# Performance work log

Hardware: AMD Instinct MI355X
Metric: run time of the kernel (lower is better)

Reference implementation:

```python
import jax, jax.numpy as jnp
import numpy as np

B, S, HID = 2, 2048, 1024
NH, HD = 4, 256
SCALE = HD ** -0.5


def _rope(x, fr, fi):
    # x: [B,S,NH,HD]; fr/fi: [S,HD//2]
    b, s, n, d = x.shape
    xr = x.reshape(b, s, n, d // 2, 2)
    re, im = xr[..., 0], xr[..., 1]
    fr = fr[None, :, None, :]
    fi = fi[None, :, None, :]
    rr = re * fr - im * fi
    ri = re * fi + im * fr
    return jnp.stack((rr, ri), axis=-1).reshape(b, s, n, d)


def setup_inputs() -> dict:
    key = jax.random.key(0)
    k1, k2, k3 = jax.random.split(key, 3)
    hidden_states = jax.random.normal(k1, (B, S, HID), dtype=jnp.float32)
    # RoPE frequencies (standard theta=10000)
    inv_freq = 1.0 / (10000.0 ** (np.arange(0, HD, 2, dtype=np.float32) / HD))  # [HD//2]
    t = np.arange(S, dtype=np.float32)
    ang = np.outer(t, inv_freq)  # [S, HD//2]
    freqs_real = jnp.asarray(np.cos(ang), dtype=jnp.float32)
    freqs_imag = jnp.asarray(np.sin(ang), dtype=jnp.float32)
    # causal additive mask [1,1,S,S]
    causal = jnp.tril(jnp.ones((S, S), dtype=bool))
    mask = jnp.where(causal, 0.0, -1e9).astype(jnp.float32)[None, None]
    W_qkv = jax.random.normal(k2, (3 * HID, HID), dtype=jnp.float32) * (HID ** -0.5)
    W_o = jax.random.normal(k3, (HID, HID), dtype=jnp.float32) * (HID ** -0.5)
    return {"hidden_states": hidden_states, "freqs_real": freqs_real,
            "freqs_imag": freqs_imag, "mask": mask, "W_qkv": W_qkv, "W_o": W_o}


def reference(hidden_states, freqs_real, freqs_imag, mask, W_qkv, W_o):
    b, s, _ = hidden_states.shape
    qkv = hidden_states @ W_qkv.T  # [B,S,3*HID]
    qkv = qkv.reshape(b, s, 3, NH, HD)
    q, k, v = qkv[:, :, 0], qkv[:, :, 1], qkv[:, :, 2]
    q = _rope(q, freqs_real, freqs_imag)
    k = _rope(k, freqs_real, freqs_imag)
    scores = jnp.einsum('bqhd,bkhd->bhqk', q * SCALE, k) + mask  # [B,NH,S,S]
    probs = jax.nn.softmax(scores, axis=-1)
    attn = jnp.einsum('bhqk,bkhd->bqhd', probs, v).reshape(b, s, HID)
    return attn @ W_o.T
```

## Files before the change

### kernel.cpp

```cpp
#include <hip/hip_runtime.h>
#include <stdint.h>

#define NB 2
#define NS 2048
#define NHID 1024
#define NHEADS 4
#define DHEAD 256
#define NP 128
#define QK_SCALE 0.0625f

typedef unsigned short ushort_t;
typedef __bf16 bf16x8 __attribute__((ext_vector_type(8)));
typedef float floatx4 __attribute__((ext_vector_type(4)));
typedef short shortx8 __attribute__((ext_vector_type(8)));
typedef unsigned short ushortx4 __attribute__((ext_vector_type(4)));
typedef unsigned short ushortx8 __attribute__((ext_vector_type(8)));

__device__ __forceinline__ float bf2f(ushort_t u) {
    unsigned int x = ((unsigned int)u) << 16;
    return __builtin_bit_cast(float, x);
}
__device__ __forceinline__ ushort_t f2bf(float f) {
    unsigned int u = __builtin_bit_cast(unsigned int, f);
    u += 0x7fff + ((u >> 16) & 1);
    return (ushort_t)(u >> 16);
}

__device__ __forceinline__ floatx4 mfma16(bf16x8 a, bf16x8 b, floatx4 c) {
    return __builtin_amdgcn_mfma_f32_16x16x32_bf16(a, b, c, 0, 0, 0);
}

__device__ __forceinline__ void gload_lds16(const void* g, void* l) {
    __builtin_amdgcn_global_load_lds(
        (const __attribute__((address_space(1))) void*)g,
        (__attribute__((address_space(3))) void*)l, 16, 0, 0);
}

#define N4_H (4096 * 1024 / 4)
#define N4_WQ (3072 * 1024 / 4)
#define N4_WO (1024 * 1024 / 4)
__global__ __launch_bounds__(256) void cast3_kernel(const float* __restrict__ inH,
                                                    const float* __restrict__ inWq,
                                                    const float* __restrict__ inWo,
                                                    ushort_t* __restrict__ out) {
    int i = blockIdx.x * 256 + threadIdx.x;
    const float* src;
    int j = i;
    if (i < N4_H) {
        src = inH;
    } else if (i < N4_H + N4_WQ) {
        src = inWq; j = i - N4_H;
    } else {
        src = inWo; j = i - (N4_H + N4_WQ);
    }
    float4 v = ((const float4*)src)[j];
    ushortx4 o = { f2bf(v.x), f2bf(v.y), f2bf(v.z), f2bf(v.w) };
    ((ushortx4*)out)[i] = o;
}


__global__ __launch_bounds__(256) void gemm_bt_f32s(const ushort_t* __restrict__ A,
                                                    const ushort_t* __restrict__ Bt,
                                                    float* __restrict__ C0,
                                                    float* __restrict__ C1,
                                                    int M, int N, int K) {
    __shared__ ushort_t sA[4][128 * 32];
    __shared__ ushort_t sB[4][128 * 32];
    const int t = threadIdx.x;
    const int f = blockIdx.x;
    const int xcd = f & 7;
    const int idx = f >> 3;
    const int im = idx >> 4;
    const int in = (idx >> 1) & 7;
    const int kz = idx & 1;
    const int m0 = (xcd * 4 + im) * 128;
    const int n0 = in * 128;
    float* Cout = kz ? C1 : C0;
    const int kbeg = kz * (K / 2);
    const int w = t >> 6, l = t & 63;
    const int wm = (w >> 1) * 64, wn = (w & 1) * 64;
    const int lc = l & 15, lq = l >> 4;

    floatx4 acc[4][4];
#pragma unroll
    for (int i = 0; i < 4; i++)
#pragma unroll
        for (int j = 0; j < 4; j++) acc[i][j] = (floatx4){0.f, 0.f, 0.f, 0.f};

    const int srow = w * 16 + (l >> 2);
    const int scol = (((l & 3) - (l >> 2)) & 3) * 8;
    const ushort_t* Ag = A + (size_t)(m0 + srow) * K + scol + kbeg;
    const ushort_t* Bg = Bt + (size_t)(n0 + srow) * K + scol + kbeg;
    const int lofs = t * 8;

    auto stage = [&](int bsel, int kk) {
        ushort_t* lA = &sA[bsel][lofs];
        ushort_t* lB = &sB[bsel][lofs];
        gload_lds16(Ag + kk, lA);
        gload_lds16(Ag + kk + (size_t)64 * K, lA + 2048);
        gload_lds16(Bg + kk, lB);
        gload_lds16(Bg + kk + (size_t)64 * K, lB + 2048);
    };
    auto compute = [&](int bsel) {
        const ushort_t* cA = sA[bsel];
        const ushort_t* cB = sB[bsel];
        bf16x8 af[4], bfv[4];
#pragma unroll
        for (int i = 0; i < 4; i++) {
            int R = wm + i * 16 + lc;
            af[i] = *(const bf16x8*)&cA[R * 32 + ((lq + R) & 3) * 8];
        }
#pragma unroll
        for (int j = 0; j < 4; j++) {
            int R = wn + j * 16 + lc;
            bfv[j] = *(const bf16x8*)&cB[R * 32 + ((lq + R) & 3) * 8];
        }
#pragma unroll
        for (int i = 0; i < 4; i++)
#pragma unroll
            for (int j = 0; j < 4; j++)
                acc[i][j] = mfma16(af[i], bfv[j], acc[i][j]);
    };

    stage(0, 0); stage(1, 32); stage(2, 64);
#pragma unroll 1
    for (int s = 0; s <= 16 - 4; ++s) {
        asm volatile("s_waitcnt vmcnt(8)" ::: "memory");
        __builtin_amdgcn_sched_barrier(0);
        __builtin_amdgcn_s_barrier();
        compute(s & 3);
        stage((s + 3) & 3, (s + 3) * 32);
    }
    asm volatile("s_waitcnt vmcnt(8)" ::: "memory");
    __builtin_amdgcn_sched_barrier(0);
    __builtin_amdgcn_s_barrier();
    compute(13 & 3);
    asm volatile("s_waitcnt vmcnt(4)" ::: "memory");
    __builtin_amdgcn_sched_barrier(0);
    __builtin_amdgcn_s_barrier();
    compute(14 & 3);
    asm volatile("s_waitcnt vmcnt(0)" ::: "memory");
    __builtin_amdgcn_sched_barrier(0);
    __builtin_amdgcn_s_barrier();
    compute(15 & 3);

#pragma unroll
    for (int i = 0; i < 4; i++) {
        int row = m0 + wm + i * 16 + lq * 4;
#pragma unroll
        for (int j = 0; j < 4; j++) {
            int col = n0 + wn + j * 16 + lc;
#pragma unroll
            for (int r = 0; r < 4; r++)
                Cout[(size_t)(row + r) * N + col] = acc[i][j][r];
        }
    }
}

__global__ __launch_bounds__(256) void add_f32(const float* __restrict__ a,
                                               const float* __restrict__ b,
                                               float* __restrict__ o, int n4) {
    int i = blockIdx.x * 256 + threadIdx.x;
    if (i < n4) {
        float4 x = ((const float4*)a)[i];
        float4 y = ((const float4*)b)[i];
        float4 z = { x.x + y.x, x.y + y.y, x.z + y.z, x.w + y.w };
        ((float4*)o)[i] = z;
    }
}

__global__ __launch_bounds__(256) void gemm_qkv(const ushort_t* __restrict__ A,
                                                const ushort_t* __restrict__ Bt,
                                                const float* __restrict__ fre,
                                                const float* __restrict__ fim,
                                                ushort_t* __restrict__ Q,
                                                ushort_t* __restrict__ Kk,
                                                ushort_t* __restrict__ Vt) {
    const int M_K = 1024;
    __shared__ ushort_t sA[4][128 * 32];
    __shared__ ushort_t sB[4][128 * 32];
    const int t = threadIdx.x;
    const int f = blockIdx.x;
    const int xcd = f & 7;
    const int idx = f >> 3;
    const int mr = xcd & 3, nr = xcd >> 2;
    const int im = idx & 7, in = idx >> 3;
    const int m0 = (mr * 8 + im) * 128;
    const int n0 = (nr * 12 + in) * 128;
    const int w = t >> 6, l = t & 63;
    const int wm = (w >> 1) * 64, wn = (w & 1) * 64;
    const int lc = l & 15, lq = l >> 4;

    floatx4 acc[4][4];
#pragma unroll
    for (int i = 0; i < 4; i++)
#pragma unroll
        for (int j = 0; j < 4; j++) acc[i][j] = (floatx4){0.f, 0.f, 0.f, 0.f};

    const int srow = w * 16 + (l >> 2);
    const int scol = (((l & 3) - (l >> 2)) & 3) * 8;
    const ushort_t* Ag = A + (size_t)(m0 + srow) * M_K + scol;
    const ushort_t* Bg = Bt + (size_t)(n0 + srow) * M_K + scol;
    const int lofs = t * 8;

    auto stage = [&](int bsel, int kk) {
        ushort_t* lA = &sA[bsel][lofs];
        ushort_t* lB = &sB[bsel][lofs];
        gload_lds16(Ag + kk, lA);
        gload_lds16(Ag + kk + (size_t)64 * M_K, lA + 2048);
        gload_lds16(Bg + kk, lB);
        gload_lds16(Bg + kk + (size_t)64 * M_K, lB + 2048);
    };
    auto compute = [&](int bsel) {
        const ushort_t* cA = sA[bsel];
        const ushort_t* cB = sB[bsel];
        bf16x8 af[4], bfv[4];
#pragma unroll
        for (int i = 0; i < 4; i++) {
            int R = wm + i * 16 + lc;
            af[i] = *(const bf16x8*)&cA[R * 32 + ((lq + R) & 3) * 8];
        }
#pragma unroll
        for (int j = 0; j < 4; j++) {
            int R = wn + j * 16 + lc;
            bfv[j] = *(const bf16x8*)&cB[R * 32 + ((lq + R) & 3) * 8];
        }
#pragma unroll
        for (int i = 0; i < 4; i++)
#pragma unroll
            for (int j = 0; j < 4; j++)
                acc[i][j] = mfma16(af[i], bfv[j], acc[i][j]);
    };

    stage(0, 0); stage(1, 32); stage(2, 64);
#pragma unroll 1
    for (int s = 0; s <= 32 - 4; ++s) {
        asm volatile("s_waitcnt vmcnt(8)" ::: "memory");
        __builtin_amdgcn_sched_barrier(0);
        __builtin_amdgcn_s_barrier();
        compute(s & 3);
        stage((s + 3) & 3, (s + 3) * 32);
    }
    asm volatile("s_waitcnt vmcnt(8)" ::: "memory");
    __builtin_amdgcn_sched_barrier(0);
    __builtin_amdgcn_s_barrier();
    compute(29 & 3);
    asm volatile("s_waitcnt vmcnt(4)" ::: "memory");
    __builtin_amdgcn_sched_barrier(0);
    __builtin_amdgcn_s_barrier();
    compute(30 & 3);
    asm volatile("s_waitcnt vmcnt(0)" ::: "memory");
    __builtin_amdgcn_sched_barrier(0);
    __builtin_amdgcn_s_barrier();
    compute(31 & 3);

    const int sect = n0 >> 10;
#pragma unroll
    for (int i = 0; i < 4; i++) {
        int row = m0 + wm + i * 16 + lq * 4;
        int b = row >> 11;
        int srow2 = row & 2047;
#pragma unroll
        for (int j = 0; j < 4; j++) {
            int col = n0 + wn + j * 16 + lc;
            int d = col & 255;
            int h = (col >> 8) & 3;
            int bh = b * NHEADS + h;
            if (sect == 2) {
                ushortx4 pack = { f2bf(acc[i][j][0]), f2bf(acc[i][j][1]),
                                  f2bf(acc[i][j][2]), f2bf(acc[i][j][3]) };
                *(ushortx4*)&Vt[((size_t)bh * 256 + d) * NS + srow2] = pack;
            } else {
                int p = d >> 1;
                int odd = d & 1;
                ushort_t* dst = (sect == 0) ? Q : Kk;
#pragma unroll
                for (int r = 0; r < 4; r++) {
                    float v = acc[i][j][r];
                    float vp = __shfl_xor(v, 1);
                    int s = srow2 + r;
                    float c = fre[s * NP + p], si = fim[s * NP + p];
                    float out = odd ? (vp * si + v * c) : (v * c - vp * si);
                    if (sect == 0) out *= QK_SCALE;
                    dst[((size_t)bh * NS + s) * DHEAD + d] = f2bf(out);
                }
            }
        }
    }
}

#define BQ3 128
#define BKV3 64
#define PPAD 72
#define CHCAP 6
#define NPART_BH 51
#define OPART_SPLIT 224

__global__ __launch_bounds__(256, 2) void flash_attn4(const ushort_t* __restrict__ Q,
                                                      const ushort_t* __restrict__ K,
                                                      const ushort_t* __restrict__ Vt,
                                                      ushort_t* __restrict__ OpA,
                                                      ushort_t* __restrict__ OpB,
                                                      float* __restrict__ ml) {
    __shared__ ushort_t sK[BKV3 * 256];
    __shared__ ushort_t sV[DHEAD * 64];
    __shared__ ushort_t sP[4][16 * PPAD];

    int rem = blockIdx.x, qt = 15, nsp;
    for (;;) {
        nsp = (2 * (qt + 1) + CHCAP - 1) / CHCAP;
        if (rem < nsp) break;
        rem -= nsp;
        qt--;
    }
    const int nch = 2 * (qt + 1);
    const int cbeg = rem * CHCAP;
    const int cend = (cbeg + CHCAP < nch) ? cbeg + CHCAP : nch;

    const int h = blockIdx.y, b = blockIdx.z;
    const int t = threadIdx.x, w = t >> 6, l = t & 63;
    const int lc = l & 15, lq = l >> 4;
    const int bh = b * NHEADS + h;
    const size_t base = (size_t)bh * NS * DHEAD;
    const int q0 = qt * BQ3;

    const int krb = w * 2 + (l >> 5);
    const int kck = ((l & 31) - (krb & 7)) & 31;
    const size_t koff = (size_t)krb * 256 + kck * 8;
    const int vrb = w * 8 + (l >> 3);
    const int vck = ((l & 7) - (vrb & 7)) & 7;
    const size_t voff = (size_t)vrb * NS + vck * 8;
    ushort_t* dK = &sK[w * 512 + l * 8];
    ushort_t* dV = &sV[w * 512 + l * 8];

    bf16x8 qf[2][8];
#pragma unroll
    for (int gq = 0; gq < 2; gq++) {
        const ushort_t* qrow = Q + base + (size_t)(q0 + w * 32 + gq * 16 + lc) * DHEAD + lq * 8;
#pragma unroll
        for (int dk = 0; dk < 8; dk++) qf[gq][dk] = *(const bf16x8*)(qrow + dk * 32);
    }

    floatx4 accO[2][16];
#pragma unroll
    for (int gq = 0; gq < 2; gq++)
#pragma unroll
        for (int j = 0; j < 16; j++) accO[gq][j] = (floatx4){0.f, 0.f, 0.f, 0.f};
    float lrun[2][4] = {{0.f, 0.f, 0.f, 0.f}, {0.f, 0.f, 0.f, 0.f}};

    for (int kc = cbeg; kc < cend; kc++) {
        const int kb = kc * BKV3;
        __syncthreads();
        {
            const ushort_t* ksrc = K + base + (size_t)kb * 256 + koff;
            const ushort_t* vsrc = Vt + base + kb + voff;
#pragma unroll
            for (int j = 0; j < 8; j++)
                gload_lds16(ksrc + j * (8 * 256), dK + j * 2048);
#pragma unroll
            for (int j = 0; j < 8; j++)
                gload_lds16(vsrc + j * (32 * NS), dV + j * 2048);
        }
        __syncthreads();

        floatx4 sfr[2][4];
#pragma unroll
        for (int gq = 0; gq < 2; gq++)
#pragma unroll
            for (int g = 0; g < 4; g++) sfr[gq][g] = (floatx4){0.f, 0.f, 0.f, 0.f};
#pragma unroll
        for (int dk = 0; dk < 8; dk++) {
#pragma unroll
            for (int g = 0; g < 4; g++) {
                int R = g * 16 + lc;
                int phys = (dk * 4 + lq + (R & 7)) & 31;
                bf16x8 bk = *(const bf16x8*)&sK[R * 256 + phys * 8];
                sfr[0][g] = mfma16(qf[0][dk], bk, sfr[0][g]);
                sfr[1][g] = mfma16(qf[1][dk], bk, sfr[1][g]);
            }
        }

        if (kc >= nch - 2) {
#pragma unroll
            for (int gq = 0; gq < 2; gq++)
#pragma unroll
                for (int g = 0; g < 4; g++) {
                    int kg = kb + g * 16 + lc;
                    int qr = q0 + w * 32 + gq * 16 + lq * 4;
#pragma unroll
                    for (int r = 0; r < 4; r++)
                        if (kg > qr + r) sfr[gq][g][r] = -1e30f;
                }
        }

        ushort_t* pw = sP[w];
#pragma unroll
        for (int gq = 0; gq < 2; gq++) {
#pragma unroll
            for (int g = 0; g < 4; g++)
#pragma unroll
                for (int r = 0; r < 4; r++) {
                    float p = __expf(sfr[gq][g][r]);
                    lrun[gq][r] += p;
                    pw[(lq * 4 + r) * PPAD + g * 16 + lc] = f2bf(p);
                }
            bf16x8 ap0 = *(const bf16x8*)&pw[lc * PPAD + lq * 8];
            bf16x8 ap1 = *(const bf16x8*)&pw[lc * PPAD + 32 + lq * 8];
#pragma unroll
            for (int j = 0; j < 16; j++) {
                int D = j * 16 + lc;
                int ph0 = (lq + (D & 7)) & 7;
                int ph1 = (4 + lq + (D & 7)) & 7;
                bf16x8 bv0 = *(const bf16x8*)&sV[D * 64 + ph0 * 8];
                bf16x8 bv1 = *(const bf16x8*)&sV[D * 64 + ph1 * 8];
                accO[gq][j] = mfma16(ap0, bv0, accO[gq][j]);
                accO[gq][j] = mfma16(ap1, bv1, accO[gq][j]);
            }
        }
    }

    const int pid = bh * NPART_BH + blockIdx.x;
    ushort_t* op = (pid < OPART_SPLIT) ? OpA + (size_t)pid * (128 * 256)
                                       : OpB + (size_t)(pid - OPART_SPLIT) * (128 * 256);
#pragma unroll
    for (int gq = 0; gq < 2; gq++) {
#pragma unroll
        for (int r = 0; r < 4; r++) {
            int row = w * 32 + gq * 16 + lq * 4 + r;
#pragma unroll
            for (int j = 0; j < 16; j++)
                op[row * 256 + j * 16 + lc] = f2bf(accO[gq][j][r]);
            float lv = lrun[gq][r];
#pragma unroll
            for (int off = 1; off < 16; off <<= 1) lv += __shfl_xor(lv, off);
            if (lc == 0) ml[(size_t)pid * 128 + row] = lv;
        }
    }
}

__global__ __launch_bounds__(256) void combine_parts2(const ushort_t* __restrict__ OpA,
                                                      const ushort_t* __restrict__ OpB,
                                                      const float* __restrict__ ml,
                                                      ushort_t* __restrict__ O) {
    const int qt = blockIdx.x >> 3, rsub = blockIdx.x & 7;
    const int h = blockIdx.y, b = blockIdx.z;
    const int bh = b * NHEADS + h;
    int bbase = 0;
    for (int q = 15; q > qt; q--) bbase += (2 * (q + 1) + CHCAP - 1) / CHCAP;
    const int nsp = (2 * (qt + 1) + CHCAP - 1) / CHCAP;
    const int pid0 = bh * NPART_BH + bbase;

    const int t = threadIdx.x;
    const int rl = t >> 4;
    const int c0 = (t & 15) * 16;
    const int row = rsub * 16 + rl;

    float so[16];
#pragma unroll
    for (int k = 0; k < 16; k++) so[k] = 0.f;
    float sl = 0.f;

    for (int i = 0; i < nsp; i++) {
        int pid = pid0 + i;
        const ushort_t* op = (pid < OPART_SPLIT)
                                 ? OpA + (size_t)pid * (128 * 256)
                                 : OpB + (size_t)(pid - OPART_SPLIT) * (128 * 256);
        const ushort_t* p = op + row * 256 + c0;
        ushortx8 a0 = *(const ushortx8*)p;
        ushortx8 a1 = *(const ushortx8*)(p + 8);
#pragma unroll
        for (int k = 0; k < 8; k++) {
            so[k] += bf2f(a0[k]);
            so[8 + k] += bf2f(a1[k]);
        }
        sl += ml[(size_t)pid * 128 + row];
    }

    float inv = 1.f / sl;
    ushortx8 o0, o1;
#pragma unroll
    for (int k = 0; k < 8; k++) {
        o0[k] = f2bf(so[k] * inv);
        o1[k] = f2bf(so[8 + k] * inv);
    }
    int s = qt * BQ3 + row;
    ushort_t* dst = O + ((size_t)(b * NS + s) * NHEADS + h) * DHEAD + c0;
    *(ushortx8*)dst = o0;
    *(ushortx8*)(dst + 8) = o1;
}

extern "C" void kernel_launch(void* const* d_in, const int* in_sizes, int n_in,
                              void* d_out, int out_size, void* d_ws, size_t ws_size,
                              hipStream_t stream) {
    const float* hidden = (const float*)d_in[0];
    const float* fre = (const float*)d_in[1];
    const float* fim = (const float*)d_in[2];
    const float* Wqkv = (const float*)d_in[4];
    const float* Wo = (const float*)d_in[5];

    char* ws = (char*)d_ws;
    ushort_t* hb    = (ushort_t*)(ws);
    ushort_t* wqkvb = (ushort_t*)(ws + 8388608);
    ushort_t* wob   = (ushort_t*)(ws + 14680064);
    ushort_t* qb    = (ushort_t*)(ws + 16777216);
    ushort_t* kb    = (ushort_t*)(ws + 25165824);
    ushort_t* vtb   = (ushort_t*)(ws + 33554432);
    ushort_t* OpA   = (ushort_t*)(ws);
    ushort_t* OpB   = (ushort_t*)(ws + 41943040);
    ushort_t* oattn = (ushort_t*)(ws + 16777216);
    float*    gP0   = (float*)(ws + 25165824);
    float*    gP1   = (float*)(ws + 41943040);
    float*    ml    = (float*)(ws + 58720256);

    cast3_kernel<<<(N4_H + N4_WQ + N4_WO) / 256, 256, 0, stream>>>(hidden, Wqkv, Wo, hb);

    gemm_qkv<<<dim3(768), 256, 0, stream>>>(
        hb, wqkvb, fre, fim, qb, kb, vtb);

    flash_attn4<<<dim3(NPART_BH, NHEADS, NB), 256, 0, stream>>>(qb, kb, vtb, OpA, OpB, ml);
    combine_parts2<<<dim3(128, NHEADS, NB), 256, 0, stream>>>(OpA, OpB, ml, oattn);

    gemm_bt_f32s<<<dim3(512), 256, 0, stream>>>(
        oattn, wob, gP0, gP1, 4096, 1024, 1024);
    add_f32<<<4096, 256, 0, stream>>>(gP0, gP1, (float*)d_out, 4096 * 1024 / 4);
}
```

Baseline: 209.2 us.

## Rewrite QKV GEMM with 256x256 tiles, 8 waves, and interleaved quarter-stage pipeline

```diff
diff --git a/kernel.cpp b/kernel.cpp
--- a/kernel.cpp
+++ b/kernel.cpp
@@ -57,7 +57,6 @@
     ushortx4 o = { f2bf(v.x), f2bf(v.y), f2bf(v.z), f2bf(v.w) };
     ((ushortx4*)out)[i] = o;
 }
-
 
 __global__ __launch_bounds__(256) void gemm_bt_f32s(const ushort_t* __restrict__ A,
                                                     const ushort_t* __restrict__ Bt,
@@ -88,7 +87,7 @@
         for (int j = 0; j < 4; j++) acc[i][j] = (floatx4){0.f, 0.f, 0.f, 0.f};
 
     const int srow = w * 16 + (l >> 2);
-    const int scol = (((l & 3) - (l >> 2)) & 3) * 8;
+    const int scol = (((l & 3) - (l >> 2) - (l >> 4)) & 3) * 8;
     const ushort_t* Ag = A + (size_t)(m0 + srow) * K + scol + kbeg;
     const ushort_t* Bg = Bt + (size_t)(n0 + srow) * K + scol + kbeg;
     const int lofs = t * 8;
@@ -108,12 +107,12 @@
 #pragma unroll
         for (int i = 0; i < 4; i++) {
             int R = wm + i * 16 + lc;
-            af[i] = *(const bf16x8*)&cA[R * 32 + ((lq + R) & 3) * 8];
+            af[i] = *(const bf16x8*)&cA[R * 32 + ((lq + R + (R >> 2)) & 3) * 8];
         }
 #pragma unroll
         for (int j = 0; j < 4; j++) {
             int R = wn + j * 16 + lc;
-            bfv[j] = *(const bf16x8*)&cB[R * 32 + ((lq + R) & 3) * 8];
+            bfv[j] = *(const bf16x8*)&cB[R * 32 + ((lq + R + (R >> 2)) & 3) * 8];
         }
 #pragma unroll
         for (int i = 0; i < 4; i++)
@@ -169,103 +168,133 @@
     }
 }
 
-__global__ __launch_bounds__(256) void gemm_qkv(const ushort_t* __restrict__ A,
-                                                const ushort_t* __restrict__ Bt,
-                                                const float* __restrict__ fre,
-                                                const float* __restrict__ fim,
-                                                ushort_t* __restrict__ Q,
-                                                ushort_t* __restrict__ Kk,
-                                                ushort_t* __restrict__ Vt) {
-    const int M_K = 1024;
-    __shared__ ushort_t sA[4][128 * 32];
-    __shared__ ushort_t sB[4][128 * 32];
+#define WAITV(n) do { asm volatile("s_waitcnt vmcnt(" #n ")" ::: "memory"); \
+                      __builtin_amdgcn_sched_barrier(0); } while (0)
+#define WAITL    do { asm volatile("s_waitcnt lgkmcnt(0)" ::: "memory"); \
+                      __builtin_amdgcn_sched_barrier(0); } while (0)
+
+#define STAGE_A(nb, half, kk) do { \
+    gload_lds16(Ab + (size_t)((half) * 128) * 1024 + (kk), &sA[nb][(half) * 8192 + ldst]); \
+    gload_lds16(Ab + (size_t)((half) * 128 + 64) * 1024 + (kk), &sA[nb][(half) * 8192 + 4096 + ldst]); \
+} while (0)
+#define STAGE_B(nb, half, kk) do { \
+    gload_lds16(Bb + (size_t)((half) * 128) * 1024 + (kk), &sB[nb][(half) * 8192 + ldst]); \
+    gload_lds16(Bb + (size_t)((half) * 128 + 64) * 1024 + (kk), &sB[nb][(half) * 8192 + 4096 + ldst]); \
+} while (0)
+
+#define LOAD_A(cA, mh) do { \
+    _Pragma("unroll") \
+    for (int ii = 0; ii < 4; ii++) { \
+        const int R = wrm + (mh) * 64 + ii * 16 + lc; \
+        af[ii][0] = *(const bf16x8*)&(cA)[R * 64 + ((lq + R) & 7) * 8]; \
+        af[ii][1] = *(const bf16x8*)&(cA)[R * 64 + ((4 + lq + R) & 7) * 8]; \
+    } \
+} while (0)
+#define LOAD_B(cB, nh) do { \
+    _Pragma("unroll") \
+    for (int jj = 0; jj < 2; jj++) { \
+        const int R = wcn + (nh) * 32 + jj * 16 + lc; \
+        bfr[jj][0] = *(const bf16x8*)&(cB)[R * 64 + ((lq + R) & 7) * 8]; \
+        bfr[jj][1] = *(const bf16x8*)&(cB)[R * 64 + ((4 + lq + R) & 7) * 8]; \
+    } \
+} while (0)
+#define MMA(mh, nh) do { \
+    _Pragma("unroll") \
+    for (int ii = 0; ii < 4; ii++) \
+    _Pragma("unroll") \
+    for (int jj = 0; jj < 2; jj++) { \
+        acc[(mh) * 4 + ii][(nh) * 2 + jj] = \
+            mfma16(af[ii][0], bfr[jj][0], acc[(mh) * 4 + ii][(nh) * 2 + jj]); \
+        acc[(mh) * 4 + ii][(nh) * 2 + jj] = \
+            mfma16(af[ii][1], bfr[jj][1], acc[(mh) * 4 + ii][(nh) * 2 + jj]); \
+    } \
+} while (0)
+
+__global__ __launch_bounds__(512, 2) void gemm_qkv(const ushort_t* __restrict__ A,
+                                                   const ushort_t* __restrict__ Bt,
+                                                   const float* __restrict__ fre,
+                                                   const float* __restrict__ fim,
+                                                   ushort_t* __restrict__ Q,
+                                                   ushort_t* __restrict__ Kk,
+                                                   ushort_t* __restrict__ Vt) {
+    __shared__ ushort_t sA[2][256 * 64];
+    __shared__ ushort_t sB[2][256 * 64];
     const int t = threadIdx.x;
     const int f = blockIdx.x;
     const int xcd = f & 7;
     const int idx = f >> 3;
-    const int mr = xcd & 3, nr = xcd >> 2;
-    const int im = idx & 7, in = idx >> 3;
-    const int m0 = (mr * 8 + im) * 128;
-    const int n0 = (nr * 12 + in) * 128;
+    const int im = idx & 1, in = idx >> 1;
+    const int m0 = (xcd * 2 + im) * 256;
+    const int n0 = in * 256;
     const int w = t >> 6, l = t & 63;
-    const int wm = (w >> 1) * 64, wn = (w & 1) * 64;
+    const int wr = w >> 2, wc = w & 3;
+    const int wrm = wr * 128, wcn = wc * 64;
     const int lc = l & 15, lq = l >> 4;
 
-    floatx4 acc[4][4];
-#pragma unroll
-    for (int i = 0; i < 4; i++)
+    floatx4 acc[8][4];
+#pragma unroll
+    for (int i = 0; i < 8; i++)
 #pragma unroll
         for (int j = 0; j < 4; j++) acc[i][j] = (floatx4){0.f, 0.f, 0.f, 0.f};
 
-    const int srow = w * 16 + (l >> 2);
-    const int scol = (((l & 3) - (l >> 2)) & 3) * 8;
-    const ushort_t* Ag = A + (size_t)(m0 + srow) * M_K + scol;
-    const ushort_t* Bg = Bt + (size_t)(n0 + srow) * M_K + scol;
-    const int lofs = t * 8;
-
-    auto stage = [&](int bsel, int kk) {
-        ushort_t* lA = &sA[bsel][lofs];
-        ushort_t* lB = &sB[bsel][lofs];
-        gload_lds16(Ag + kk, lA);
-        gload_lds16(Ag + kk + (size_t)64 * M_K, lA + 2048);
-        gload_lds16(Bg + kk, lB);
-        gload_lds16(Bg + kk + (size_t)64 * M_K, lB + 2048);
-    };
-    auto compute = [&](int bsel) {
-        const ushort_t* cA = sA[bsel];
-        const ushort_t* cB = sB[bsel];
-        bf16x8 af[4], bfv[4];
-#pragma unroll
-        for (int i = 0; i < 4; i++) {
-            int R = wm + i * 16 + lc;
-            af[i] = *(const bf16x8*)&cA[R * 32 + ((lq + R) & 3) * 8];
-        }
+    const int arow = t >> 3;
+    const int ac8 = ((((t & 7) - (arow & 7)) & 7)) * 8;
+    const ushort_t* Ab = A + (size_t)(m0 + arow) * 1024 + ac8;
+    const ushort_t* Bb = Bt + (size_t)(n0 + arow) * 1024 + ac8;
+    const int ldst = t * 8;
+
+    STAGE_A(0, 1, 0); STAGE_B(0, 0, 0); STAGE_A(0, 0, 0); STAGE_B(0, 1, 0);
+
+#pragma unroll 1
+    for (int kt = 0; kt < 16; ++kt) {
+        const int b = kt & 1, nb = b ^ 1;
+        const ushort_t* cA = sA[b];
+        const ushort_t* cB = sB[b];
+        const int kn = (kt < 15 ? kt + 1 : 15) * 64;
+        bf16x8 af[4][2], bfr[2][2];
+
+        WAITV(2);
+        __builtin_amdgcn_s_barrier();
+        LOAD_A(cA, 0); LOAD_B(cB, 0);
+        STAGE_A(nb, 1, kn);
+        WAITL;
+        __builtin_amdgcn_s_setprio(1); MMA(0, 0); __builtin_amdgcn_s_setprio(0);
+
+        WAITV(2);
+        __builtin_amdgcn_s_barrier();
+        LOAD_B(cB, 1);
+        STAGE_B(nb, 0, kn);
+        WAITL;
+        __builtin_amdgcn_s_setprio(1); MMA(0, 1); __builtin_amdgcn_s_setprio(0);
+
+        WAITV(4);
+        __builtin_amdgcn_s_barrier();
+        LOAD_A(cA, 1);
+        STAGE_A(nb, 0, kn);
+        WAITL;
+        __builtin_amdgcn_s_setprio(1); MMA(1, 1); __builtin_amdgcn_s_setprio(0);
+
+        WAITV(6);
+        __builtin_amdgcn_s_barrier();
+        LOAD_B(cB, 0);
+        STAGE_B(nb, 1, kn);
+        WAITL;
+        __builtin_amdgcn_s_setprio(1); MMA(1, 0); __builtin_amdgcn_s_setprio(0);
+    }
+    asm volatile("s_waitcnt vmcnt(0)" ::: "memory");
+
+    const int sect = n0 >> 10;
+#pragma unroll
+    for (int i = 0; i < 8; i++) {
+        int row = m0 + wrm + i * 16 + lq * 4;
+        int bb = row >> 11;
+        int srow2 = row & 2047;
 #pragma unroll
         for (int j = 0; j < 4; j++) {
-            int R = wn + j * 16 + lc;
-            bfv[j] = *(const bf16x8*)&cB[R * 32 + ((lq + R) & 3) * 8];
-        }
-#pragma unroll
-        for (int i = 0; i < 4; i++)
-#pragma unroll
-            for (int j = 0; j < 4; j++)
-                acc[i][j] = mfma16(af[i], bfv[j], acc[i][j]);
-    };
-
-    stage(0, 0); stage(1, 32); stage(2, 64);
-#pragma unroll 1
-    for (int s = 0; s <= 32 - 4; ++s) {
-        asm volatile("s_waitcnt vmcnt(8)" ::: "memory");
-        __builtin_amdgcn_sched_barrier(0);
-        __builtin_amdgcn_s_barrier();
-        compute(s & 3);
-        stage((s + 3) & 3, (s + 3) * 32);
-    }
-    asm volatile("s_waitcnt vmcnt(8)" ::: "memory");
-    __builtin_amdgcn_sched_barrier(0);
-    __builtin_amdgcn_s_barrier();
-    compute(29 & 3);
-    asm volatile("s_waitcnt vmcnt(4)" ::: "memory");
-    __builtin_amdgcn_sched_barrier(0);
-    __builtin_amdgcn_s_barrier();
-    compute(30 & 3);
-    asm volatile("s_waitcnt vmcnt(0)" ::: "memory");
-    __builtin_amdgcn_sched_barrier(0);
-    __builtin_amdgcn_s_barrier();
-    compute(31 & 3);
-
-    const int sect = n0 >> 10;
-#pragma unroll
-    for (int i = 0; i < 4; i++) {
-        int row = m0 + wm + i * 16 + lq * 4;
-        int b = row >> 11;
-        int srow2 = row & 2047;
-#pragma unroll
-        for (int j = 0; j < 4; j++) {
-            int col = n0 + wn + j * 16 + lc;
+            int col = n0 + wcn + j * 16 + lc;
             int d = col & 255;
             int h = (col >> 8) & 3;
-            int bh = b * NHEADS + h;
+            int bh = bb * NHEADS + h;
             if (sect == 2) {
                 ushortx4 pack = { f2bf(acc[i][j][0]), f2bf(acc[i][j][1]),
                                   f2bf(acc[i][j][2]), f2bf(acc[i][j][3]) };
@@ -514,7 +543,7 @@
 
     cast3_kernel<<<(N4_H + N4_WQ + N4_WO) / 256, 256, 0, stream>>>(hidden, Wqkv, Wo, hb);
 
-    gemm_qkv<<<dim3(768), 256, 0, stream>>>(
+    gemm_qkv<<<dim3(192), 512, 0, stream>>>(
         hb, wqkvb, fre, fim, qb, kb, vtb);
 
     flash_attn4<<<dim3(NPART_BH, NHEADS, NB), 256, 0, stream>>>(qb, kb, vtb, OpA, OpB, ml);
```

Result: no change. 205.3 us (-1.9%).

## Enlarge QKV GEMM tiles to 256x256 with 512 threads and new LDS swizzle

Applied to the files above, without the earlier changes.

```diff
diff --git a/kernel.cpp b/kernel.cpp
--- a/kernel.cpp
+++ b/kernel.cpp
@@ -57,7 +57,6 @@
     ushortx4 o = { f2bf(v.x), f2bf(v.y), f2bf(v.z), f2bf(v.w) };
     ((ushortx4*)out)[i] = o;
 }
-
 
 __global__ __launch_bounds__(256) void gemm_bt_f32s(const ushort_t* __restrict__ A,
                                                     const ushort_t* __restrict__ Bt,
@@ -88,7 +87,7 @@
         for (int j = 0; j < 4; j++) acc[i][j] = (floatx4){0.f, 0.f, 0.f, 0.f};
 
     const int srow = w * 16 + (l >> 2);
-    const int scol = (((l & 3) - (l >> 2)) & 3) * 8;
+    const int scol = (((l & 3) - (l >> 2) - (l >> 4)) & 3) * 8;
     const ushort_t* Ag = A + (size_t)(m0 + srow) * K + scol + kbeg;
     const ushort_t* Bg = Bt + (size_t)(n0 + srow) * K + scol + kbeg;
     const int lofs = t * 8;
@@ -108,12 +107,12 @@
 #pragma unroll
         for (int i = 0; i < 4; i++) {
             int R = wm + i * 16 + lc;
-            af[i] = *(const bf16x8*)&cA[R * 32 + ((lq + R) & 3) * 8];
+            af[i] = *(const bf16x8*)&cA[R * 32 + ((lq + R + (R >> 2)) & 3) * 8];
         }
 #pragma unroll
         for (int j = 0; j < 4; j++) {
             int R = wn + j * 16 + lc;
-            bfv[j] = *(const bf16x8*)&cB[R * 32 + ((lq + R) & 3) * 8];
+            bfv[j] = *(const bf16x8*)&cB[R * 32 + ((lq + R + (R >> 2)) & 3) * 8];
         }
 #pragma unroll
         for (int i = 0; i < 4; i++)
@@ -128,20 +127,24 @@
         asm volatile("s_waitcnt vmcnt(8)" ::: "memory");
         __builtin_amdgcn_sched_barrier(0);
         __builtin_amdgcn_s_barrier();
+        asm volatile("" ::: "memory");
         compute(s & 3);
         stage((s + 3) & 3, (s + 3) * 32);
     }
     asm volatile("s_waitcnt vmcnt(8)" ::: "memory");
     __builtin_amdgcn_sched_barrier(0);
     __builtin_amdgcn_s_barrier();
+    asm volatile("" ::: "memory");
     compute(13 & 3);
     asm volatile("s_waitcnt vmcnt(4)" ::: "memory");
     __builtin_amdgcn_sched_barrier(0);
     __builtin_amdgcn_s_barrier();
+    asm volatile("" ::: "memory");
     compute(14 & 3);
     asm volatile("s_waitcnt vmcnt(0)" ::: "memory");
     __builtin_amdgcn_sched_barrier(0);
     __builtin_amdgcn_s_barrier();
+    asm volatile("" ::: "memory");
     compute(15 & 3);
 
 #pragma unroll
@@ -169,103 +172,102 @@
     }
 }
 
-__global__ __launch_bounds__(256) void gemm_qkv(const ushort_t* __restrict__ A,
-                                                const ushort_t* __restrict__ Bt,
-                                                const float* __restrict__ fre,
-                                                const float* __restrict__ fim,
-                                                ushort_t* __restrict__ Q,
-                                                ushort_t* __restrict__ Kk,
-                                                ushort_t* __restrict__ Vt) {
-    const int M_K = 1024;
-    __shared__ ushort_t sA[4][128 * 32];
-    __shared__ ushort_t sB[4][128 * 32];
+__global__ __launch_bounds__(512, 2) void gemm_qkv(const ushort_t* __restrict__ A,
+                                                   const ushort_t* __restrict__ Bt,
+                                                   const float* __restrict__ fre,
+                                                   const float* __restrict__ fim,
+                                                   ushort_t* __restrict__ Q,
+                                                   ushort_t* __restrict__ Kk,
+                                                   ushort_t* __restrict__ Vt) {
+    __shared__ ushort_t sA[4][8192];
+    __shared__ ushort_t sB[4][8192];
     const int t = threadIdx.x;
     const int f = blockIdx.x;
     const int xcd = f & 7;
     const int idx = f >> 3;
-    const int mr = xcd & 3, nr = xcd >> 2;
-    const int im = idx & 7, in = idx >> 3;
-    const int m0 = (mr * 8 + im) * 128;
-    const int n0 = (nr * 12 + in) * 128;
+    const int mreg = xcd >> 1, nreg = xcd & 1;
+    const int im = idx & 3, in = idx >> 2;
+    const int m0 = (mreg * 4 + im) * 256;
+    const int n0 = (nreg * 6 + in) * 256;
     const int w = t >> 6, l = t & 63;
-    const int wm = (w >> 1) * 64, wn = (w & 1) * 64;
+    const int wr = w >> 2, wc = w & 3;
+    const int wrm = wr * 128, wcn = wc * 64;
     const int lc = l & 15, lq = l >> 4;
 
-    floatx4 acc[4][4];
-#pragma unroll
-    for (int i = 0; i < 4; i++)
+    floatx4 acc[8][4];
+#pragma unroll
+    for (int i = 0; i < 8; i++)
 #pragma unroll
         for (int j = 0; j < 4; j++) acc[i][j] = (floatx4){0.f, 0.f, 0.f, 0.f};
 
-    const int srow = w * 16 + (l >> 2);
-    const int scol = (((l & 3) - (l >> 2)) & 3) * 8;
-    const ushort_t* Ag = A + (size_t)(m0 + srow) * M_K + scol;
-    const ushort_t* Bg = Bt + (size_t)(n0 + srow) * M_K + scol;
-    const int lofs = t * 8;
-
-    auto stage = [&](int bsel, int kk) {
-        ushort_t* lA = &sA[bsel][lofs];
-        ushort_t* lB = &sB[bsel][lofs];
-        gload_lds16(Ag + kk, lA);
-        gload_lds16(Ag + kk + (size_t)64 * M_K, lA + 2048);
-        gload_lds16(Bg + kk, lB);
-        gload_lds16(Bg + kk + (size_t)64 * M_K, lB + 2048);
+    const int srow = t >> 2;
+    const int sc8 = ((((t & 3) - (t >> 2) - (t >> 4)) & 3)) * 8;
+    const ushort_t* Ab = A + (size_t)(m0 + srow) * 1024 + sc8;
+    const ushort_t* Bb = Bt + (size_t)(n0 + srow) * 1024 + sc8;
+    const int ldst = t * 8;
+
+    auto STAGE = [&](int buf, int kk) {
+        gload_lds16(Ab + kk, &sA[buf][ldst]);
+        gload_lds16(Ab + (size_t)128 * 1024 + kk, &sA[buf][4096 + ldst]);
+        gload_lds16(Bb + kk, &sB[buf][ldst]);
+        gload_lds16(Bb + (size_t)128 * 1024 + kk, &sB[buf][4096 + ldst]);
     };
-    auto compute = [&](int bsel) {
-        const ushort_t* cA = sA[bsel];
-        const ushort_t* cB = sB[bsel];
-        bf16x8 af[4], bfv[4];
-#pragma unroll
-        for (int i = 0; i < 4; i++) {
-            int R = wm + i * 16 + lc;
-            af[i] = *(const bf16x8*)&cA[R * 32 + ((lq + R) & 3) * 8];
+    auto COMPUTE = [&](int buf) {
+        const ushort_t* cA = sA[buf];
+        const ushort_t* cB = sB[buf];
+        bf16x8 af[8], bfr[4];
+#pragma unroll
+        for (int i = 0; i < 8; i++) {
+            const int R = wrm + i * 16 + lc;
+            af[i] = *(const bf16x8*)&cA[R * 32 + ((lq + R + (R >> 2)) & 3) * 8];
         }
 #pragma unroll
         for (int j = 0; j < 4; j++) {
-            int R = wn + j * 16 + lc;
-            bfv[j] = *(const bf16x8*)&cB[R * 32 + ((lq + R) & 3) * 8];
-        }
-#pragma unroll
-        for (int i = 0; i < 4; i++)
+            const int R = wcn + j * 16 + lc;
+            bfr[j] = *(const bf16x8*)&cB[R * 32 + ((lq + R + (R >> 2)) & 3) * 8];
+        }
+        asm volatile("s_waitcnt lgkmcnt(0)" ::: "memory");
+        __builtin_amdgcn_sched_barrier(0);
+        __builtin_amdgcn_s_setprio(1);
+#pragma unroll
+        for (int i = 0; i < 8; i++)
 #pragma unroll
             for (int j = 0; j < 4; j++)
-                acc[i][j] = mfma16(af[i], bfv[j], acc[i][j]);
+                acc[i][j] = mfma16(af[i], bfr[j], acc[i][j]);
+        __builtin_amdgcn_s_setprio(0);
     };
 
-    stage(0, 0); stage(1, 32); stage(2, 64);
+#define QWAITV(n) do { asm volatile("s_waitcnt vmcnt(" #n ")" ::: "memory"); \
+                       __builtin_amdgcn_sched_barrier(0); } while (0)
+#define QBAR      do { asm volatile("" ::: "memory"); \
+                       __builtin_amdgcn_s_barrier(); \
+                       asm volatile("" ::: "memory"); } while (0)
+
+    STAGE(0, 0); STAGE(1, 32); STAGE(2, 64);
+
 #pragma unroll 1
-    for (int s = 0; s <= 32 - 4; ++s) {
-        asm volatile("s_waitcnt vmcnt(8)" ::: "memory");
-        __builtin_amdgcn_sched_barrier(0);
-        __builtin_amdgcn_s_barrier();
-        compute(s & 3);
-        stage((s + 3) & 3, (s + 3) * 32);
-    }
-    asm volatile("s_waitcnt vmcnt(8)" ::: "memory");
-    __builtin_amdgcn_sched_barrier(0);
-    __builtin_amdgcn_s_barrier();
-    compute(29 & 3);
-    asm volatile("s_waitcnt vmcnt(4)" ::: "memory");
-    __builtin_amdgcn_sched_barrier(0);
-    __builtin_amdgcn_s_barrier();
-    compute(30 & 3);
-    asm volatile("s_waitcnt vmcnt(0)" ::: "memory");
-    __builtin_amdgcn_sched_barrier(0);
-    __builtin_amdgcn_s_barrier();
-    compute(31 & 3);
+    for (int kt = 0; kt < 29; ++kt) {
+        QWAITV(8);
+        QBAR;
+        STAGE((kt + 3) & 3, (kt + 3) * 32);
+        COMPUTE(kt & 3);
+    }
+    QWAITV(8); QBAR; COMPUTE(29 & 3);
+    QWAITV(4); QBAR; COMPUTE(30 & 3);
+    QWAITV(0); QBAR; COMPUTE(31 & 3);
 
     const int sect = n0 >> 10;
 #pragma unroll
-    for (int i = 0; i < 4; i++) {
-        int row = m0 + wm + i * 16 + lq * 4;
-        int b = row >> 11;
+    for (int i = 0; i < 8; i++) {
+        int row = m0 + wrm + i * 16 + lq * 4;
+        int bb = row >> 11;
         int srow2 = row & 2047;
 #pragma unroll
         for (int j = 0; j < 4; j++) {
-            int col = n0 + wn + j * 16 + lc;
+            int col = n0 + wcn + j * 16 + lc;
             int d = col & 255;
             int h = (col >> 8) & 3;
-            int bh = b * NHEADS + h;
+            int bh = bb * NHEADS + h;
             if (sect == 2) {
                 ushortx4 pack = { f2bf(acc[i][j][0]), f2bf(acc[i][j][1]),
                                   f2bf(acc[i][j][2]), f2bf(acc[i][j][3]) };
@@ -514,7 +516,7 @@
 
     cast3_kernel<<<(N4_H + N4_WQ + N4_WO) / 256, 256, 0, stream>>>(hidden, Wqkv, Wo, hb);
 
-    gemm_qkv<<<dim3(768), 256, 0, stream>>>(
+    gemm_qkv<<<dim3(192), 512, 0, stream>>>(
         hb, wqkvb, fre, fim, qb, kb, vtb);
 
     flash_attn4<<<dim3(NPART_BH, NHEADS, NB), 256, 0, stream>>>(qb, kb, vtb, OpA, OpB, ml);
```

Measured after the change: 217.2 us. 3.8% more time.
